# Kernel tuning notes

Hardware: AMD Instinct MI355X
Metric: run time of the kernel (lower is better)

The kernel has to match this reference:

```python
import jax, jax.numpy as jnp
import numpy as np

VOCAB = 32000
HID = 2048
MAXLEN = 128


def setup_inputs() -> dict:
    key = jax.random.key(0)
    ks = jax.random.split(key, 16)
    s = 0.02
    return {
        "input_seq": jax.random.randint(ks[0], (1, 1), 0, VOCAB),
        "hidden": jax.random.normal(ks[1], (1, 1, HID), jnp.float32),
        "encoder_outputs": jax.random.normal(ks[2], (MAXLEN, HID), jnp.float32),
        "emb": jax.random.normal(ks[3], (VOCAB, HID), jnp.float32) * s,
        "attn_W": jax.random.normal(ks[4], (MAXLEN, 2 * HID), jnp.float32) * s,
        "attn_b": jnp.zeros((MAXLEN,), jnp.float32),
        "comb_W": jax.random.normal(ks[5], (HID, 2 * HID), jnp.float32) * s,
        "comb_b": jnp.zeros((HID,), jnp.float32),
        "W_ih": jax.random.normal(ks[6], (HID, HID), jnp.float32) * s,
        "W_hh": jax.random.normal(ks[7], (HID, HID), jnp.float32) * s,
        "b_ih": jnp.zeros((HID,), jnp.float32),
        "b_hh": jnp.zeros((HID,), jnp.float32),
        "out_W": jax.random.normal(ks[8], (VOCAB, HID), jnp.float32) * s,
        "out_b": jnp.zeros((VOCAB,), jnp.float32),
    }


def _rnn_step(x, h, W_ih, W_hh, b_ih, b_hh):
    # Elman RNN cell (tanh): seq_len=1 so output == new hidden. Shapes [1,1,H].
    return jnp.tanh(x @ W_ih.T + b_ih + h @ W_hh.T + b_hh)


def reference(input_seq, hidden, encoder_outputs, emb, attn_W, attn_b,
              comb_W, comb_b, W_ih, W_hh, b_ih, b_hh, out_W, out_b):
    tok = input_seq[0]                       # [1]
    x = emb[tok].reshape(1, 1, -1)           # [1,1,H]
    hidden = _rnn_step(x, hidden, W_ih, W_hh, b_ih, b_hh)   # [1,1,H]
    # second embedding of the decoder token (dropout is identity at eval)
    embedded = emb[tok].reshape(1, 1, -1)    # [1,1,H]
    attn_in = jnp.concatenate([embedded[0], hidden[0]], axis=1)   # [1,2H]
    attn_weights = jax.nn.softmax(attn_in @ attn_W.T + attn_b, axis=1)  # [1,L]
    attn_applied = attn_weights @ encoder_outputs                 # [1,H]
    o = jnp.concatenate([embedded[0], attn_applied], axis=1) @ comb_W.T + comb_b
    o = jax.nn.relu(o)[None]                 # [1,1,H]
    out_h = _rnn_step(o, hidden, W_ih, W_hh, b_ih, b_hh)          # [1,1,H]
    logits = out_h[0] @ out_W.T + out_b      # [1,VOCAB]
    return jax.nn.log_softmax(logits, axis=1)
```

## Files before the change

kernel.cpp:

```cpp
#include <hip/hip_runtime.h>
#include <math.h>

#define HID 2048
#define MAXLEN 128
#define VOCAB 32000

typedef float f4 __attribute__((ext_vector_type(4)));

__device__ __forceinline__ float wave_sum(float v) {
    #pragma unroll
    for (int m = 1; m < 64; m <<= 1) v += __shfl_xor(v, m, 64);
    return v;
}

__device__ __forceinline__ float dot4(float4 a, float4 b) {
    return a.x * b.x + a.y * b.y + a.z * b.z + a.w * b.w;
}
__device__ __forceinline__ float dot4v(f4 a, f4 b) {
    return a.x * b.x + a.y * b.y + a.z * b.z + a.w * b.w;
}

__device__ __forceinline__ float block_sum256(float v) {
    __shared__ float s[4];
    v = wave_sum(v);
    const int lane = threadIdx.x & 63, w = threadIdx.x >> 6;
    if (lane == 0) s[w] = v;
    __syncthreads();
    return s[0] + s[1] + s[2] + s[3];
}

__device__ __forceinline__ float row_dot2048(const float4* __restrict__ w,
                                             const float4* __restrict__ x) {
    const int t = threadIdx.x;
    return dot4(w[t], x[t]) + dot4(w[t + 256], x[t + 256]);
}

__global__ __launch_bounds__(256)
void k1_fused_left(const float* __restrict__ W_ih, const float* __restrict__ W_hh,
                   const float* __restrict__ emb, const int* __restrict__ tok,
                   const float* __restrict__ hidden,
                   const float* __restrict__ b_ih, const float* __restrict__ b_hh,
                   const float* __restrict__ attn_W, const float* __restrict__ attn_b,
                   const float* __restrict__ comb_W, const float* __restrict__ comb_b,
                   float* __restrict__ H1, float* __restrict__ ALe,
                   float* __restrict__ Oe) {
    const float4* xemb = (const float4*)(emb + (size_t)tok[0] * HID);
    const int bid = blockIdx.x, t = threadIdx.x;
    if (bid < HID) {
        const float4* w1 = (const float4*)(W_ih + (size_t)bid * HID);
        const float4* w2 = (const float4*)(W_hh + (size_t)bid * HID);
        float p = row_dot2048(w1, xemb) + row_dot2048(w2, (const float4*)hidden);
        p = block_sum256(p);
        if (t == 0) H1[bid] = tanhf(p + b_ih[bid] + b_hh[bid]);
    } else if (bid < HID + MAXLEN) {
        const int l = bid - HID;
        const float4* w = (const float4*)(attn_W + (size_t)l * 2 * HID);
        float p = block_sum256(row_dot2048(w, xemb));
        if (t == 0) ALe[l] = p + attn_b[l];
    } else {
        const int r = bid - HID - MAXLEN;
        const float4* w = (const float4*)(comb_W + (size_t)r * 2 * HID);
        float p = block_sum256(row_dot2048(w, xemb));
        if (t == 0) Oe[r] = p + comb_b[r];
    }
}

__global__ __launch_bounds__(256)
void k2_attn_right(const float* __restrict__ attn_W, const float* __restrict__ H1,
                   const float* __restrict__ ALe, float* __restrict__ AL) {
    const int l = blockIdx.x, t = threadIdx.x;
    const float4* w = (const float4*)(attn_W + (size_t)l * 2 * HID + HID);
    float p = block_sum256(row_dot2048(w, (const float4*)H1));
    if (t == 0) AL[l] = ALe[l] + p;
}

__global__ __launch_bounds__(256)
void k3_softmax_apply(const float* __restrict__ AL, const float* __restrict__ enc,
                      float* __restrict__ AA) {
    __shared__ float sAL[MAXLEN];
    __shared__ float wts[MAXLEN];
    __shared__ float cs[4][64];
    const int t = threadIdx.x;
    if (t < MAXLEN) sAL[t] = AL[t];
    __syncthreads();
    float m = sAL[0];
    for (int l = 1; l < MAXLEN; ++l) m = fmaxf(m, sAL[l]);
    float s = 0.f;
    for (int l = 0; l < MAXLEN; ++l) s += expf(sAL[l] - m);
    if (t < MAXLEN) wts[t] = expf(sAL[t] - m) / s;
    __syncthreads();
    const int j  = blockIdx.x * 64 + (t & 63);
    const int l0 = t >> 6;
    float acc = 0.f;
    #pragma unroll 8
    for (int l = l0; l < MAXLEN; l += 4) acc += wts[l] * enc[(size_t)l * HID + j];
    cs[l0][t & 63] = acc;
    __syncthreads();
    if (t < 64) AA[blockIdx.x * 64 + t] = cs[0][t] + cs[1][t] + cs[2][t] + cs[3][t];
}

__global__ __launch_bounds__(256)
void k4_comb_right(const float* __restrict__ comb_W, const float* __restrict__ AA,
                   const float* __restrict__ Oe, float* __restrict__ O) {
    const int r = blockIdx.x, t = threadIdx.x;
    const float4* w = (const float4*)(comb_W + (size_t)r * 2 * HID + HID);
    float p = block_sum256(row_dot2048(w, (const float4*)AA));
    if (t == 0) O[r] = fmaxf(Oe[r] + p, 0.f);
}

__global__ __launch_bounds__(256)
void k5_rnn2(const float* __restrict__ W_ih, const float* __restrict__ W_hh,
             const float* __restrict__ O, const float* __restrict__ H1,
             const float* __restrict__ b_ih, const float* __restrict__ b_hh,
             float* __restrict__ OH) {
    const int r = blockIdx.x, t = threadIdx.x;
    const float4* w1 = (const float4*)(W_ih + (size_t)r * HID);
    const float4* w2 = (const float4*)(W_hh + (size_t)r * HID);
    float p = row_dot2048(w1, (const float4*)O) + row_dot2048(w2, (const float4*)H1);
    p = block_sum256(p);
    if (t == 0) OH[r] = tanhf(p + b_ih[r] + b_hh[r]);
}

__global__ __launch_bounds__(256)
void k6_bigmv(const float* __restrict__ W, const float* __restrict__ x,
              const float* __restrict__ b, float* __restrict__ out,
              float* __restrict__ PE) {
    __shared__ float red[4];
    const int wid = threadIdx.x >> 6, lane = threadIdx.x & 63;
    const int r0 = blockIdx.x * 16 + wid * 4;
    const f4* xv = (const f4*)x;
    const f4* w0 = (const f4*)(W + (size_t)r0 * HID);
    const f4* w1 = w0 + 512;
    const f4* w2 = w0 + 1024;
    const f4* w3 = w0 + 1536;
    float a0 = 0.f, a1 = 0.f, a2 = 0.f, a3 = 0.f;
    #pragma unroll 4
    for (int k = 0; k < 8; ++k) {
        const int idx = lane + k * 64;
        const f4 xc = xv[idx];
        a0 += dot4v(w0[idx], xc);
        a1 += dot4v(w1[idx], xc);
        a2 += dot4v(w2[idx], xc);
        a3 += dot4v(w3[idx], xc);
    }
    a0 = wave_sum(a0);
    a1 = wave_sum(a1);
    a2 = wave_sum(a2);
    a3 = wave_sum(a3);
    if (lane == 0) {
        const f4 bb = *(const f4*)(b + r0);
        a0 += bb.x; a1 += bb.y; a2 += bb.z; a3 += bb.w;
        f4 o; o.x = a0; o.y = a1; o.z = a2; o.w = a3;
        *(f4*)(out + r0) = o;
        red[wid] = expf(a0) + expf(a1) + expf(a2) + expf(a3);
    }
    __syncthreads();
    if (threadIdx.x == 0) PE[blockIdx.x] = red[0] + red[1] + red[2] + red[3];
}

__global__ __launch_bounds__(256)
void k7_lse_apply(const float* __restrict__ PE, float* __restrict__ out) {
    const int t = threadIdx.x;
    float s = 0.f;
    for (int i = t; i < VOCAB / 16; i += 256) s += PE[i];
    const float lg = logf(block_sum256(s));
    out[blockIdx.x * 256 + t] -= lg;
}

extern "C" void kernel_launch(void* const* d_in, const int* in_sizes, int n_in,
                              void* d_out, int out_size, void* d_ws, size_t ws_size,
                              hipStream_t stream) {
    const int*   tok    = (const int*)  d_in[0];
    const float* hidden = (const float*)d_in[1];
    const float* enc    = (const float*)d_in[2];
    const float* emb    = (const float*)d_in[3];
    const float* attn_W = (const float*)d_in[4];
    const float* attn_b = (const float*)d_in[5];
    const float* comb_W = (const float*)d_in[6];
    const float* comb_b = (const float*)d_in[7];
    const float* W_ih   = (const float*)d_in[8];
    const float* W_hh   = (const float*)d_in[9];
    const float* b_ih   = (const float*)d_in[10];
    const float* b_hh   = (const float*)d_in[11];
    const float* out_W  = (const float*)d_in[12];
    const float* out_b  = (const float*)d_in[13];
    float* out = (float*)d_out;

    float* ws  = (float*)d_ws;
    float* H1  = ws;
    float* ALe = ws + 2048;
    float* AL  = ws + 2176;
    float* AA  = ws + 2304;
    float* Oe  = ws + 4352;
    float* O   = ws + 6400;
    float* OH  = ws + 8448;
    float* PE  = ws + 10496;

    k1_fused_left<<<HID + MAXLEN + HID, 256, 0, stream>>>(W_ih, W_hh, emb, tok, hidden,
                                                          b_ih, b_hh, attn_W, attn_b,
                                                          comb_W, comb_b, H1, ALe, Oe);
    k2_attn_right<<<MAXLEN, 256, 0, stream>>>(attn_W, H1, ALe, AL);
    k3_softmax_apply<<<HID / 64, 256, 0, stream>>>(AL, enc, AA);
    k4_comb_right<<<HID, 256, 0, stream>>>(comb_W, AA, Oe, O);
    k5_rnn2<<<HID, 256, 0, stream>>>(W_ih, W_hh, O, H1, b_ih, b_hh, OH);
    k6_bigmv<<<VOCAB / 16, 256, 0, stream>>>(out_W, OH, out_b, out, PE);
    k7_lse_apply<<<VOCAB / 256, 256, 0, stream>>>(PE, out);
}
```

Measured before the change: 86.36 us.

## Hoist second-RNN W_hh·H1 product into the attention-right kernel

The W_hh·H1 matvec for the second RNN step depends only on H1, so it moves out of k5 and into k2, which previously launched only 128 blocks and left the GPU mostly idle. k2 now runs 128+2048 blocks and k5 streams only W_ih. This shortens the serial dependency chain and fills the underused k2 launch. The cost is one extra workspace buffer and the W_hh traffic shifting into an earlier kernel.

Measured after the change: 86.09 us. About the same (-0.3%).

```diff
diff --git a/kernel.cpp b/kernel.cpp
--- a/kernel.cpp
+++ b/kernel.cpp
@@ -66,12 +66,21 @@
 }
 
 __global__ __launch_bounds__(256)
-void k2_attn_right(const float* __restrict__ attn_W, const float* __restrict__ H1,
-                   const float* __restrict__ ALe, float* __restrict__ AL) {
-    const int l = blockIdx.x, t = threadIdx.x;
-    const float4* w = (const float4*)(attn_W + (size_t)l * 2 * HID + HID);
-    float p = block_sum256(row_dot2048(w, (const float4*)H1));
-    if (t == 0) AL[l] = ALe[l] + p;
+void k2b_attn_right_hh(const float* __restrict__ attn_W, const float* __restrict__ W_hh,
+                       const float* __restrict__ H1, const float* __restrict__ ALe,
+                       float* __restrict__ AL, float* __restrict__ OHh) {
+    const int bid = blockIdx.x, t = threadIdx.x;
+    const float4* h1 = (const float4*)H1;
+    if (bid < MAXLEN) {
+        const float4* w = (const float4*)(attn_W + (size_t)bid * 2 * HID + HID);
+        float p = block_sum256(row_dot2048(w, h1));
+        if (t == 0) AL[bid] = ALe[bid] + p;
+    } else {
+        const int r = bid - MAXLEN;
+        const float4* w = (const float4*)(W_hh + (size_t)r * HID);
+        float p = block_sum256(row_dot2048(w, h1));
+        if (t == 0) OHh[r] = p;
+    }
 }
 
 __global__ __launch_bounds__(256)
@@ -109,16 +118,14 @@
 }
 
 __global__ __launch_bounds__(256)
-void k5_rnn2(const float* __restrict__ W_ih, const float* __restrict__ W_hh,
-             const float* __restrict__ O, const float* __restrict__ H1,
+void k5_rnn2(const float* __restrict__ W_ih, const float* __restrict__ O,
+             const float* __restrict__ OHh,
              const float* __restrict__ b_ih, const float* __restrict__ b_hh,
              float* __restrict__ OH) {
     const int r = blockIdx.x, t = threadIdx.x;
     const float4* w1 = (const float4*)(W_ih + (size_t)r * HID);
-    const float4* w2 = (const float4*)(W_hh + (size_t)r * HID);
-    float p = row_dot2048(w1, (const float4*)O) + row_dot2048(w2, (const float4*)H1);
-    p = block_sum256(p);
-    if (t == 0) OH[r] = tanhf(p + b_ih[r] + b_hh[r]);
+    float p = block_sum256(row_dot2048(w1, (const float4*)O));
+    if (t == 0) OH[r] = tanhf(p + OHh[r] + b_ih[r] + b_hh[r]);
 }
 
 __global__ __launch_bounds__(256)
@@ -194,15 +201,16 @@
     float* Oe  = ws + 4352;
     float* O   = ws + 6400;
     float* OH  = ws + 8448;
-    float* PE  = ws + 10496;
+    float* OHh = ws + 10496;
+    float* PE  = ws + 12544;
 
     k1_fused_left<<<HID + MAXLEN + HID, 256, 0, stream>>>(W_ih, W_hh, emb, tok, hidden,
                                                           b_ih, b_hh, attn_W, attn_b,
                                                           comb_W, comb_b, H1, ALe, Oe);
-    k2_attn_right<<<MAXLEN, 256, 0, stream>>>(attn_W, H1, ALe, AL);
+    k2b_attn_right_hh<<<MAXLEN + HID, 256, 0, stream>>>(attn_W, W_hh, H1, ALe, AL, OHh);
     k3_softmax_apply<<<HID / 64, 256, 0, stream>>>(AL, enc, AA);
     k4_comb_right<<<HID, 256, 0, stream>>>(comb_W, AA, Oe, O);
-    k5_rnn2<<<HID, 256, 0, stream>>>(W_ih, W_hh, O, H1, b_ih, b_hh, OH);
+    k5_rnn2<<<HID, 256, 0, stream>>>(W_ih, O, OHh, b_ih, b_hh, OH);
     k6_bigmv<<<VOCAB / 16, 256, 0, stream>>>(out_W, OH, out_b, out, PE);
     k7_lse_apply<<<VOCAB / 256, 256, 0, stream>>>(PE, out);
 }
```
